# Kernel optimization log

Measured on AMD Instinct MI355X. Metric: run time of the kernel, lower is better.

## Reference

```python
import jax, jax.numpy as jnp
import numpy as np

WS = 8          # window size
DIM = 192
NH = 6          # num heads
HD = DIM // NH  # head dim = 32
HIDDEN = 768    # mlp_ratio 4
EPS = 1e-5


def _rel_tables(ws):
    # continuous relative-coords table, shape (1, 2w-1, 2w-1, 2)
    r = np.arange(-(ws - 1), ws, dtype=np.float32)
    table = np.stack(np.meshgrid(r, r, indexing='ij'), axis=-1)[None]
    table = table / (ws - 1) * 8.0
    # relative position index, shape (N, N)
    coords = np.stack(np.meshgrid(np.arange(ws), np.arange(ws), indexing='ij'))
    cf = coords.reshape(2, -1)
    rel = (cf[:, :, None] - cf[:, None, :]).transpose(1, 2, 0).astype(np.int64)
    rel[:, :, 0] += ws - 1
    rel[:, :, 1] += ws - 1
    rel[:, :, 0] *= 2 * ws - 1
    idx = rel.sum(-1)
    return jnp.asarray(table), jnp.asarray(idx)

_TABLE, _RPI = _rel_tables(WS)


def _layernorm(x, g, b):
    m = jnp.mean(x, -1, keepdims=True)
    v = jnp.var(x, -1, keepdims=True)
    return (x - m) * jax.lax.rsqrt(v + EPS) * g + b


def setup_inputs() -> dict:
    key = jax.random.key(0)
    ks = jax.random.split(key, 12)
    B, H, W = 2, 256, 256
    s = 0.02
    return {
        'x': jax.random.normal(ks[0], (B, H * W, DIM), jnp.float32),
        'scale': jax.random.uniform(ks[1], (1, 2), jnp.float32, 0.5, 2.0),
        'norm1_g': jnp.ones((DIM,), jnp.float32),
        'norm1_b': jnp.zeros((DIM,), jnp.float32),
        'qkv_w': jax.random.normal(ks[2], (DIM, 3 * DIM), jnp.float32) * s,
        'qkv_b': jnp.zeros((3 * DIM,), jnp.float32),
        'proj_w': jax.random.normal(ks[3], (DIM, DIM), jnp.float32) * s,
        'proj_b': jnp.zeros((DIM,), jnp.float32),
        'cpb_w1': jax.random.normal(ks[4], (4, 512), jnp.float32) * s,
        'cpb_b1': jnp.zeros((512,), jnp.float32),
        'cpb_w2': jax.random.normal(ks[5], (512, NH), jnp.float32) * s,
        'cpb_b2': jnp.zeros((NH,), jnp.float32),
        'norm2_g': jnp.ones((DIM,), jnp.float32),
        'norm2_b': jnp.zeros((DIM,), jnp.float32),
        'fc1_w': jax.random.normal(ks[6], (DIM, HIDDEN), jnp.float32) * s,
        'fc1_b': jnp.zeros((HIDDEN,), jnp.float32),
        'fc2_w': jax.random.normal(ks[7], (HIDDEN, DIM), jnp.float32) * s,
        'fc2_b': jnp.zeros((DIM,), jnp.float32),
        'dw_w': jax.random.normal(ks[8], (HIDDEN, 1, 3, 3), jnp.float32) * s,
        'dw_b': jnp.zeros((HIDDEN,), jnp.float32),
        'H': 256,
        'W': 256,
    }


def reference(x, scale, norm1_g, norm1_b, qkv_w, qkv_b, proj_w, proj_b,
              cpb_w1, cpb_b1, cpb_w2, cpb_b2, norm2_g, norm2_b,
              fc1_w, fc1_b, fc2_w, fc2_b, dw_w, dw_b, H, W):
    B, L, C = x.shape
    N = WS * WS
    shortcut = x

    # ---- W-MSA branch ----
    h = _layernorm(x, norm1_g, norm1_b).reshape(B, H, W, C)
    # window partition -> (B*nW, N, C)
    h = h.reshape(B, H // WS, WS, W // WS, WS, C).transpose(0, 1, 3, 2, 4, 5)
    xw = h.reshape(-1, N, C)
    B_ = xw.shape[0]

    qkv = (xw @ qkv_w + qkv_b).reshape(B_, N, 3, NH, HD).transpose(2, 0, 3, 1, 4)
    q, k, v = qkv[0], qkv[1], qkv[2]          # (B_, NH, N, HD)
    q = q * (HD ** -0.5)
    attn = jnp.einsum('bhnd,bhmd->bhnm', q, k)  # (B_, NH, N, N)

    # continuous relative position bias from cpb MLP conditioned on `scale`
    rel_cell = jnp.broadcast_to(scale[:, None, None, :], _TABLE.shape)  # (1,2w-1,2w-1,2)
    coords4 = jnp.concatenate([_TABLE, rel_cell], axis=-1)              # (1,2w-1,2w-1,4)
    bias_tab = (jax.nn.relu(coords4 @ cpb_w1 + cpb_b1) @ cpb_w2 + cpb_b2).reshape(-1, NH)
    rpb = bias_tab[_RPI.reshape(-1)].reshape(N, N, NH).transpose(2, 0, 1)  # (NH,N,N)
    attn = jax.nn.softmax(attn + rpb[None], axis=-1)

    out = jnp.einsum('bhnm,bhmd->bhnd', attn, v).transpose(0, 2, 1, 3).reshape(B_, N, C)
    out = out @ proj_w + proj_b

    # window reverse
    out = out.reshape(B, H // WS, W // WS, WS, WS, C).transpose(0, 1, 3, 2, 4, 5)
    out = out.reshape(B, L, C)
    x = shortcut + out

    # ---- conv-augmented MLP branch ----
    h = _layernorm(x, norm2_g, norm2_b)
    h = jax.nn.gelu(h @ fc1_w + fc1_b, approximate=False)   # (B, L, HIDDEN)
    hc = h.transpose(0, 2, 1).reshape(B, HIDDEN, H, W)
    hc = jax.lax.conv_general_dilated(
        hc, dw_w, window_strides=(1, 1), padding=((1, 1), (1, 1)),
        dimension_numbers=('NCHW', 'OIHW', 'NCHW'), feature_group_count=HIDDEN)
    hc = hc + dw_b[None, :, None, None]
    h = hc.reshape(B, HIDDEN, L).transpose(0, 2, 1)
    h = jax.nn.gelu(h, approximate=False)
    h = h @ fc2_w + fc2_b
    return x + h
```

## Files before the change

### kernel.cpp

```cpp
#include <hip/hip_runtime.h>
#include <hip/hip_bf16.h>

typedef __attribute__((ext_vector_type(8))) short  bf16x8;
typedef __attribute__((ext_vector_type(4))) float  f32x4;
typedef __attribute__((ext_vector_type(8))) unsigned short u16x8;
typedef __attribute__((ext_vector_type(4))) unsigned short u16x4;

__device__ __forceinline__ unsigned short f2b(float f) {
    unsigned int u = __builtin_bit_cast(unsigned int, f);
    u += 0x7FFFu + ((u >> 16) & 1u);
    return (unsigned short)(u >> 16);
}
__device__ __forceinline__ float b2f(unsigned short u) {
    return __builtin_bit_cast(float, (unsigned int)u << 16);
}
__device__ __forceinline__ float gelu_fast(float x) {
    float d = 1.0f + __expf(-1.702f * x);
    return x * __builtin_amdgcn_rcpf(d);
}
__device__ __forceinline__ int wperm(int m) {
    int w = m >> 6, n = m & 63;
    int b = w >> 10, wy = (w >> 5) & 31, wx = w & 31;
    int y = wy * 8 + (n >> 3), xx = wx * 8 + (n & 7);
    return (b << 16) + (y << 8) + xx;
}
__device__ __forceinline__ int wperm_inv(int r) {
    int rb = r >> 16, ry = (r >> 8) & 255, rx = r & 255;
    return (((rb << 10) + ((ry >> 3) << 5) + (rx >> 3)) << 6) + ((ry & 7) << 3) + (rx & 7);
}

__device__ __forceinline__ void gload_lds16(const void* g, void* l) {
    __builtin_amdgcn_global_load_lds(
        (const __attribute__((address_space(1))) void*)g,
        (__attribute__((address_space(3))) void*)l, 16, 0, 0);
}

__global__ void transpose_w(const float* __restrict__ in, unsigned short* __restrict__ out,
                            int K, int N) {
    int i = blockIdx.x * 256 + threadIdx.x;
    if (i >= K * N) return;
    int n = i / K, k = i - n * K;
    out[i] = f2b(in[k * N + n]);
}

__global__ void transpose_wf(const float* __restrict__ in, float* __restrict__ out,
                             int K, int N) {
    int i = blockIdx.x * 256 + threadIdx.x;
    if (i >= K * N) return;
    int n = i / K, k = i - n * K;
    out[i] = in[k * N + n];
}

__global__ __launch_bounds__(256) void cpb_kernel(
    const float* __restrict__ scale, const float* __restrict__ w1, const float* __restrict__ b1,
    const float* __restrict__ w2, const float* __restrict__ b2, float* __restrict__ btab) {
    int t = threadIdx.x;
    if (t >= 225) return;
    int i = t / 15, j = t - (t / 15) * 15;
    float ti = (i - 7) * (8.0f / 7.0f);
    float tj = (j - 7) * (8.0f / 7.0f);
    float s0 = scale[0], s1 = scale[1];
    float acc[6];
    #pragma unroll
    for (int h = 0; h < 6; ++h) acc[h] = b2[h];
    for (int k = 0; k < 512; ++k) {
        float hv = ti * w1[k] + tj * w1[512 + k] + s0 * w1[1024 + k] + s1 * w1[1536 + k] + b1[k];
        hv = fmaxf(hv, 0.f);
        #pragma unroll
        for (int h = 0; h < 6; ++h) acc[h] += hv * w2[k * 6 + h];
    }
    #pragma unroll
    for (int h = 0; h < 6; ++h) btab[t * 6 + h] = acc[h];
}

__global__ __launch_bounds__(256) void ln_full(
    const float* __restrict__ xin, const float* __restrict__ g, const float* __restrict__ b,
    unsigned short* __restrict__ ow) {
    int r = blockIdx.x * 4 + (threadIdx.x >> 6);
    int lane = threadIdx.x & 63;
    const float* p = xin + (size_t)r * 192;
    float a0 = p[lane], a1 = p[lane + 64], a2 = p[lane + 128];
    float s = a0 + a1 + a2;
    float q = a0 * a0 + a1 * a1 + a2 * a2;
    #pragma unroll
    for (int off = 1; off < 64; off <<= 1) {
        s += __shfl_xor(s, off);
        q += __shfl_xor(q, off);
    }
    float mean = s * (1.f / 192.f);
    float rstd = rsqrtf(q * (1.f / 192.f) - mean * mean + 1e-5f);
    unsigned short* o = ow + (size_t)wperm_inv(r) * 192;
    o[lane]       = f2b((a0 - mean) * rstd * g[lane] + b[lane]);
    o[lane + 64]  = f2b((a1 - mean) * rstd * g[lane + 64] + b[lane + 64]);
    o[lane + 128] = f2b((a2 - mean) * rstd * g[lane + 128] + b[lane + 128]);
}

template<int MODE>
__global__ __launch_bounds__(256) void gemm192(
    const float* __restrict__ Af, const unsigned short* __restrict__ Ab,
    const float* __restrict__ stats, const float* __restrict__ lng, const float* __restrict__ lnb,
    const unsigned short* __restrict__ Bt, const float* __restrict__ bias,
    unsigned short* __restrict__ oq, unsigned short* __restrict__ ok2, unsigned short* __restrict__ ov,
    const float* __restrict__ resid, float* __restrict__ ofp, unsigned short* __restrict__ obf,
    float* __restrict__ ostat) {
    __shared__ __align__(16) unsigned short Asw[2 * 128 * 64];
    __shared__ __align__(16) unsigned short Bsw[2 * 192 * 64];
    const int t = threadIdx.x;
    const int lane = t & 63;
    const int wv = t >> 6, wm = wv >> 1, wn = wv & 1;
    const int n0 = blockIdx.x * 192;
    const int m0 = blockIdx.y * 128;
    const int l15 = lane & 15, lq = lane >> 4;

    int aoffs[4], boffs[6];
    if constexpr (MODE != 2) {
        #pragma unroll
        for (int s = 0; s < 4; ++s) {
            int row = (wv + 4 * s) * 8 + (lane >> 3);
            aoffs[s] = (m0 + row) * 192 + (((lane & 7) ^ (lane >> 3)) * 8);
        }
    }
    #pragma unroll
    for (int s = 0; s < 6; ++s) {
        int row = (wv + 4 * s) * 8 + (lane >> 3);
        boffs[s] = (n0 + row) * 192 + (((lane & 7) ^ (lane >> 3)) * 8);
    }

    f32x4 acc[4][6];
    #pragma unroll
    for (int i = 0; i < 4; ++i)
        #pragma unroll
        for (int j = 0; j < 6; ++j) acc[i][j] = (f32x4){0.f, 0.f, 0.f, 0.f};

    if constexpr (MODE != 2) {
        #pragma unroll
        for (int s = 0; s < 4; ++s)
            gload_lds16(Ab + aoffs[s], (char*)Asw + (wv + 4 * s) * 1024);
    }
    #pragma unroll
    for (int s = 0; s < 6; ++s)
        gload_lds16(Bt + boffs[s], (char*)Bsw + (wv + 4 * s) * 1024);

    int cur = 0;
    const int axor = (l15 & 7) << 4;
    for (int c = 0; c < 3; ++c) {
        const int k0 = c * 64;
        if (c < 2) {
            if constexpr (MODE != 2) {
                #pragma unroll
                for (int s = 0; s < 4; ++s)
                    gload_lds16(Ab + aoffs[s] + k0 + 64,
                                (char*)Asw + (cur ^ 1) * 16384 + (wv + 4 * s) * 1024);
            }
            #pragma unroll
            for (int s = 0; s < 6; ++s)
                gload_lds16(Bt + boffs[s] + k0 + 64,
                            (char*)Bsw + (cur ^ 1) * 24576 + (wv + 4 * s) * 1024);
        }
        if constexpr (MODE == 2) {
            #pragma unroll
            for (int i = 0; i < 8; ++i) {
                int c2 = t + i * 256;
                int row = c2 >> 4, ch = c2 & 15;
                int m = m0 + row;
                f32x4 v = *(const f32x4*)(Af + (size_t)m * 192 + k0 + ch * 4);
                float mean = stats[2 * m], rstd = stats[2 * m + 1];
                u16x4 pk;
                #pragma unroll
                for (int j = 0; j < 4; ++j) {
                    int kk = k0 + ch * 4 + j;
                    pk[j] = f2b((v[j] - mean) * rstd * lng[kk] + lnb[kk]);
                }
                int byte = row * 128 + ((((ch >> 1) ^ (row & 7)) << 4) + ((ch & 1) << 3));
                *(u16x4*)((char*)Asw + byte) = pk;
            }
            asm volatile("s_waitcnt lgkmcnt(0)" ::: "memory");
        }
        if (c < 2) {
            if constexpr (MODE == 2) asm volatile("s_waitcnt vmcnt(6)" ::: "memory");
            else                     asm volatile("s_waitcnt vmcnt(10)" ::: "memory");
        } else {
            asm volatile("s_waitcnt vmcnt(0)" ::: "memory");
        }
        __builtin_amdgcn_s_barrier();
        __builtin_amdgcn_sched_barrier(0);
        const char* Al = (const char*)Asw + ((MODE == 2) ? 0 : cur * 16384);
        const char* Bl = (const char*)Bsw + cur * 24576;
        #pragma unroll
        for (int kk = 0; kk < 2; ++kk) {
            bf16x8 a[4], bb[6];
            #pragma unroll
            for (int mt = 0; mt < 4; ++mt)
                a[mt] = *(const bf16x8*)(Al + (wm * 64 + mt * 16 + l15) * 128 +
                                         ((kk << 6) ^ (lq << 4) ^ axor));
            #pragma unroll
            for (int nt = 0; nt < 6; ++nt)
                bb[nt] = *(const bf16x8*)(Bl + (wn * 96 + nt * 16 + l15) * 128 +
                                          ((kk << 6) ^ (lq << 4) ^ axor));
            #pragma unroll
            for (int mt = 0; mt < 4; ++mt)
                #pragma unroll
                for (int nt = 0; nt < 6; ++nt)
                    acc[mt][nt] = __builtin_amdgcn_mfma_f32_16x16x32_bf16(a[mt], bb[nt], acc[mt][nt], 0, 0, 0);
        }
        __builtin_amdgcn_sched_barrier(0);
        __builtin_amdgcn_s_barrier();
        __builtin_amdgcn_sched_barrier(0);
        cur ^= 1;
    }

    if constexpr (MODE == 1) {
        float* ls  = (float*)Asw;
        float* lsq = ls + 256;
        #pragma unroll
        for (int mt = 0; mt < 4; ++mt) {
            #pragma unroll
            for (int r = 0; r < 4; ++r) {
                int lrow = wm * 64 + mt * 16 + lq * 4 + r;
                int m = m0 + lrow;
                int r2 = wperm(m);
                float s = 0.f, q = 0.f;
                #pragma unroll
                for (int nt = 0; nt < 6; ++nt) {
                    int c = wn * 96 + nt * 16 + l15;
                    size_t idx = (size_t)r2 * 192 + c;
                    float w = resid[idx] + acc[mt][nt][r] + bias[c];
                    ofp[idx] = w;
                    s += w;
                    q += w * w;
                }
                #pragma unroll
                for (int off = 1; off < 16; off <<= 1) {
                    s += __shfl_xor(s, off);
                    q += __shfl_xor(q, off);
                }
                if (l15 == 0) {
                    ls[lrow * 2 + wn] = s;
                    lsq[lrow * 2 + wn] = q;
                }
            }
        }
        __syncthreads();
        if (t < 128) {
            float s = ls[t * 2] + ls[t * 2 + 1];
            float q = lsq[t * 2] + lsq[t * 2 + 1];
            float mean = s * (1.f / 192.f);
            float var = q * (1.f / 192.f) - mean * mean;
            int r2 = wperm(m0 + t);
            ostat[2 * r2] = mean;
            ostat[2 * r2 + 1] = rsqrtf(var + 1e-5f);
        }
    } else {
        #pragma unroll
        for (int mt = 0; mt < 4; ++mt) {
            #pragma unroll
            for (int nt = 0; nt < 6; ++nt) {
                #pragma unroll
                for (int r = 0; r < 4; ++r) {
                    int m = m0 + wm * 64 + mt * 16 + lq * 4 + r;
                    int c = n0 + wn * 96 + nt * 16 + l15;
                    float v = acc[mt][nt][r] + bias[c];
                    if constexpr (MODE == 0) {
                        int which = c / 192;
                        int head = (c % 192) >> 5;
                        int d = c & 31;
                        int w = m >> 6, n = m & 63;
                        unsigned short* dst = (which == 0) ? oq : (which == 1) ? ok2 : ov;
                        if (which == 0) v *= 0.17677669529663689f;
                        dst[((size_t)(w * 6 + head) * 64 + n) * 32 + d] = f2b(v);
                    } else {
                        obf[(size_t)m * 768 + c] = f2b(gelu_fast(v));
                    }
                }
            }
        }
    }
}

__global__ __launch_bounds__(64) void attn_win(
    const unsigned short* __restrict__ qb, const unsigned short* __restrict__ kb,
    const unsigned short* __restrict__ vb, const float* __restrict__ btab,
    unsigned short* __restrict__ ao) {
    __shared__ float sb[225];
    __shared__ __align__(16) unsigned short pl[64 * 72];
    __shared__ __align__(16) unsigned short vT[32 * 72];
    const int bid = blockIdx.x;
    const int w = bid / 6, h = bid - w * 6;
    const int lane = threadIdx.x;
    const int l15 = lane & 15, lq = lane >> 4;

    for (int i = lane; i < 225; i += 64) sb[i] = btab[i * 6 + h];

    const unsigned short* qp = qb + (size_t)bid * 2048;
    const unsigned short* kp = kb + (size_t)bid * 2048;
    const unsigned short* vp = vb + (size_t)bid * 2048;

    bf16x8 qf[4], kf[4];
    #pragma unroll
    for (int i = 0; i < 4; ++i) {
        qf[i] = *(const bf16x8*)(qp + (i * 16 + l15) * 32 + lq * 8);
        kf[i] = *(const bf16x8*)(kp + (i * 16 + l15) * 32 + lq * 8);
    }
    #pragma unroll
    for (int i = 0; i < 4; ++i) {
        int c = lane + i * 64;
        int mr = c >> 2, d0 = (c & 3) * 8;
        u16x8 v = *(const u16x8*)(vp + mr * 32 + d0);
        #pragma unroll
        for (int j = 0; j < 8; ++j) vT[(d0 + j) * 72 + mr] = v[j];
    }
    f32x4 s[4][4];
    #pragma unroll
    for (int mt = 0; mt < 4; ++mt)
        #pragma unroll
        for (int nt = 0; nt < 4; ++nt)
            s[mt][nt] = __builtin_amdgcn_mfma_f32_16x16x32_bf16(
                qf[mt], kf[nt], (f32x4){0.f, 0.f, 0.f, 0.f}, 0, 0, 0);
    __syncthreads();
    #pragma unroll
    for (int mt = 0; mt < 4; ++mt) {
        #pragma unroll
        for (int r = 0; r < 4; ++r) {
            int n = mt * 16 + lq * 4 + r;
            int ny = n >> 3, nx = n & 7;
            float sv[4];
            float mx = -1e30f;
            #pragma unroll
            for (int nt = 0; nt < 4; ++nt) {
                int m = nt * 16 + l15;
                int idx = (ny - (m >> 3) + 7) * 15 + (nx - (m & 7) + 7);
                float val = s[mt][nt][r] + sb[idx];
                sv[nt] = val;
                mx = fmaxf(mx, val);
            }
            #pragma unroll
            for (int off = 1; off < 16; off <<= 1) mx = fmaxf(mx, __shfl_xor(mx, off));
            float sum = 0.f;
            #pragma unroll
            for (int nt = 0; nt < 4; ++nt) { sv[nt] = __expf(sv[nt] - mx); sum += sv[nt]; }
            #pragma unroll
            for (int off = 1; off < 16; off <<= 1) sum += __shfl_xor(sum, off);
            float inv = 1.f / sum;
            #pragma unroll
            for (int nt = 0; nt < 4; ++nt)
                pl[n * 72 + nt * 16 + l15] = f2b(sv[nt] * inv);
        }
    }
    __syncthreads();
    f32x4 o[4][2];
    #pragma unroll
    for (int i = 0; i < 4; ++i)
        #pragma unroll
        for (int j = 0; j < 2; ++j) o[i][j] = (f32x4){0.f, 0.f, 0.f, 0.f};
    #pragma unroll
    for (int mt = 0; mt < 4; ++mt)
        #pragma unroll
        for (int kk = 0; kk < 2; ++kk) {
            bf16x8 a = *(bf16x8*)&pl[(mt * 16 + l15) * 72 + kk * 32 + lq * 8];
            #pragma unroll
            for (int dt = 0; dt < 2; ++dt) {
                bf16x8 b = *(bf16x8*)&vT[(dt * 16 + l15) * 72 + kk * 32 + lq * 8];
                o[mt][dt] = __builtin_amdgcn_mfma_f32_16x16x32_bf16(a, b, o[mt][dt], 0, 0, 0);
            }
        }
    #pragma unroll
    for (int mt = 0; mt < 4; ++mt)
        #pragma unroll
        for (int dt = 0; dt < 2; ++dt)
            #pragma unroll
            for (int r = 0; r < 4; ++r) {
                int n = mt * 16 + lq * 4 + r;
                int d = dt * 16 + l15;
                ao[((size_t)w * 64 + n) * 192 + h * 32 + d] = f2b(o[mt][dt][r]);
            }
}

__global__ __launch_bounds__(512) void conv_fc2_v12(
    const unsigned short* __restrict__ m1, const float* __restrict__ dwwTf,
    const float* __restrict__ dwb, const unsigned short* __restrict__ fc2T,
    const float* __restrict__ fc2b, float* __restrict__ out) {
    __shared__ __align__(16) unsigned short Xs[4 * 34 * 64];
    __shared__ __align__(16) unsigned short As[64 * 72];
    __shared__ __align__(16) unsigned short Bsw[192 * 64];
    const int t = threadIdx.x;
    const int g = ((blockIdx.x & 7) << 8) + (blockIdx.x >> 3);
    const int b = g >> 10, ypair = (g >> 3) & 127, xq = g & 7;
    const int y0 = ypair * 2, x0 = xq * 32;
    const int cg = t & 7, lx = t >> 3;
    const int ix = lx & 31, iy = lx >> 5;
    const size_t ibase = (size_t)b * 65536;

    const int lane = t & 63, wv8 = t >> 6;
    const int wm = wv8 >> 2, wn = wv8 & 3;
    const int l15 = lane & 15, lq = lane >> 4;

    int xoff[3];
    #pragma unroll
    for (int s = 0; s < 3; ++s) {
        int seg = (s < 2) ? (wv8 + 8 * s) : 16;
        int p = seg * 8 + (lane >> 3);
        int ry = p / 34, px = p - ry * 34;
        int gy = min(max(y0 - 1 + ry, 0), 255);
        int gx = min(max(x0 - 1 + px, 0), 255);
        xoff[s] = ((b << 16) + (gy << 8) + gx) * 768 + (lane & 7) * 8;
    }
    int boff[3];
    #pragma unroll
    for (int s = 0; s < 3; ++s) {
        int row = (wv8 + 8 * s) * 8 + (lane >> 3);
        boff[s] = row * 768 + ((lane & 7) ^ (lane >> 3)) * 8;
    }

    f32x4 acc[2][3];
    #pragma unroll
    for (int i = 0; i < 2; ++i)
        #pragma unroll
        for (int j = 0; j < 3; ++j) acc[i][j] = (f32x4){0.f, 0.f, 0.f, 0.f};

    #pragma unroll
    for (int s = 0; s < 3; ++s)
        if (s < 2 || wv8 == 0)
            gload_lds16(m1 + xoff[s], (char*)Xs + (((s < 2) ? (wv8 + 8 * s) : 16)) * 1024);
    #pragma unroll
    for (int s = 0; s < 3; ++s)
        gload_lds16(fc2T + boff[s], (char*)Bsw + (wv8 + 8 * s) * 1024);

    const int xb = ix * 128 + cg * 16;
    const int gxp = x0 + ix;
    const bool xok0 = gxp >= 1;
    const bool xok2 = gxp <= 254;
    const int oy = y0 + iy;
    const int o00 = (lq * 16) ^ ((l15 & 7) << 4);
    const int brow = (wn * 48 + l15) * 128;

    for (int k0 = 0; k0 < 768; k0 += 64) {
        const int c0 = k0 + cg * 8;
        asm volatile("s_waitcnt vmcnt(0)" ::: "memory");
        __syncthreads();
        float a[8];
        #pragma unroll
        for (int j = 0; j < 8; ++j) a[j] = 0.f;
        #pragma unroll
        for (int ky = 0; ky < 3; ++ky) {
            if ((unsigned)(oy + ky - 1) >= 256u) continue;
            #pragma unroll
            for (int kx = 0; kx < 3; ++kx) {
                if (kx == 0 && !xok0) continue;
                if (kx == 2 && !xok2) continue;
                const float* wp = dwwTf + (ky * 3 + kx) * 768 + c0;
                f32x4 w0 = *(const f32x4*)wp;
                f32x4 w1 = *(const f32x4*)(wp + 4);
                u16x8 in = *(const u16x8*)((const char*)Xs + (iy + ky) * 4352 + xb + kx * 128);
                #pragma unroll
                for (int j = 0; j < 4; ++j) {
                    a[j]     += b2f(in[j]) * w0[j];
                    a[4 + j] += b2f(in[4 + j]) * w1[j];
                }
            }
        }
        {
            f32x4 b0 = *(const f32x4*)(dwb + c0);
            f32x4 b1 = *(const f32x4*)(dwb + c0 + 4);
            u16x8 o;
            #pragma unroll
            for (int j = 0; j < 4; ++j) {
                o[j]     = f2b(gelu_fast(a[j] + b0[j]));
                o[4 + j] = f2b(gelu_fast(a[4 + j] + b1[j]));
            }
            *(u16x8*)&As[lx * 72 + cg * 8] = o;
        }
        __syncthreads();
        if (k0 < 704) {
            #pragma unroll
            for (int s = 0; s < 3; ++s)
                if (s < 2 || wv8 == 0)
                    gload_lds16(m1 + xoff[s] + k0 + 64,
                                (char*)Xs + (((s < 2) ? (wv8 + 8 * s) : 16)) * 1024);
        }
        #pragma unroll
        for (int kk = 0; kk < 2; ++kk) {
            bf16x8 af[2];
            #pragma unroll
            for (int mt = 0; mt < 2; ++mt)
                af[mt] = *(bf16x8*)&As[(wm * 32 + mt * 16 + l15) * 72 + kk * 32 + lq * 8];
            #pragma unroll
            for (int nt = 0; nt < 3; ++nt) {
                bf16x8 bb = *(const bf16x8*)((const char*)Bsw + brow + nt * 2048 + (o00 ^ (kk << 6)));
                #pragma unroll
                for (int mt = 0; mt < 2; ++mt)
                    acc[mt][nt] = __builtin_amdgcn_mfma_f32_16x16x32_bf16(af[mt], bb, acc[mt][nt], 0, 0, 0);
            }
        }
        __syncthreads();
        if (k0 < 704) {
            #pragma unroll
            for (int s = 0; s < 3; ++s)
                gload_lds16(fc2T + boff[s] + k0 + 64, (char*)Bsw + (wv8 + 8 * s) * 1024);
        }
    }
    #pragma unroll
    for (int mt = 0; mt < 2; ++mt)
        #pragma unroll
        for (int nt = 0; nt < 3; ++nt)
            #pragma unroll
            for (int r = 0; r < 4; ++r) {
                int ml = wm * 32 + mt * 16 + lq * 4 + r;
                int py = ml >> 5, lxx = ml & 31;
                int col = wn * 48 + nt * 16 + l15;
                size_t idx = (ibase + (size_t)(y0 + py) * 256 + x0 + lxx) * 192 + col;
                out[idx] = out[idx] + acc[mt][nt][r] + fc2b[col];
            }
}

extern "C" void kernel_launch(void* const* d_in, const int* in_sizes, int n_in,
                              void* d_out, int out_size, void* d_ws, size_t ws_size,
                              hipStream_t stream) {
    (void)in_sizes; (void)n_in; (void)out_size; (void)ws_size;
    const float* x     = (const float*)d_in[0];
    const float* scale = (const float*)d_in[1];
    const float* n1g   = (const float*)d_in[2];
    const float* n1b   = (const float*)d_in[3];
    const float* qkvw  = (const float*)d_in[4];
    const float* qkvb  = (const float*)d_in[5];
    const float* projw = (const float*)d_in[6];
    const float* projb = (const float*)d_in[7];
    const float* cw1   = (const float*)d_in[8];
    const float* cb1   = (const float*)d_in[9];
    const float* cw2   = (const float*)d_in[10];
    const float* cb2   = (const float*)d_in[11];
    const float* n2g   = (const float*)d_in[12];
    const float* n2b   = (const float*)d_in[13];
    const float* fc1w  = (const float*)d_in[14];
    const float* fc1b  = (const float*)d_in[15];
    const float* fc2w  = (const float*)d_in[16];
    const float* fc2b  = (const float*)d_in[17];
    const float* dww   = (const float*)d_in[18];
    const float* dwb   = (const float*)d_in[19];
    float* out = (float*)d_out;

    char* ws = (char*)d_ws;
    unsigned short* qkvT  = (unsigned short*)ws;
    unsigned short* projT = qkvT + 110592;
    unsigned short* fc1T  = projT + 36864;
    unsigned short* fc2T  = fc1T + 147456;
    float* btab   = (float*)(ws + 1048576);
    float* dwwTf  = (float*)(ws + 1310720);
    float* stats  = (float*)(ws + 2097152);
    unsigned short* pool = (unsigned short*)(ws + 4194304);
    const size_t S = 25165824;
    unsigned short* qb = pool;
    unsigned short* kb = pool + S;
    unsigned short* vb = pool + 2 * S;
    unsigned short* ab = pool + 3 * S;
    unsigned short* m1 = pool;
    unsigned short* xnw = (unsigned short*)d_out;

    transpose_w<<<432, 256, 0, stream>>>(qkvw, qkvT, 192, 576);
    transpose_w<<<144, 256, 0, stream>>>(projw, projT, 192, 192);
    transpose_w<<<576, 256, 0, stream>>>(fc1w, fc1T, 192, 768);
    transpose_w<<<576, 256, 0, stream>>>(fc2w, fc2T, 768, 192);
    transpose_wf<<<27, 256, 0, stream>>>(dww, dwwTf, 768, 9);
    cpb_kernel<<<1, 256, 0, stream>>>(scale, cw1, cb1, cw2, cb2, btab);

    ln_full<<<32768, 256, 0, stream>>>(x, n1g, n1b, xnw);
    gemm192<0><<<dim3(3, 1024), 256, 0, stream>>>(
        (const float*)nullptr, xnw, (const float*)nullptr, (const float*)nullptr,
        (const float*)nullptr, qkvT, qkvb,
        qb, kb, vb, (const float*)nullptr, (float*)nullptr, (unsigned short*)nullptr,
        (float*)nullptr);
    attn_win<<<12288, 64, 0, stream>>>(qb, kb, vb, btab, ab);
    gemm192<1><<<dim3(1, 1024), 256, 0, stream>>>(
        (const float*)nullptr, ab, (const float*)nullptr, (const float*)nullptr,
        (const float*)nullptr, projT, projb,
        (unsigned short*)nullptr, (unsigned short*)nullptr, (unsigned short*)nullptr,
        x, out, (unsigned short*)nullptr, stats);
    gemm192<2><<<dim3(4, 1024), 256, 0, stream>>>(
        out, (const unsigned short*)nullptr, stats, n2g, n2b, fc1T, fc1b,
        (unsigned short*)nullptr, (unsigned short*)nullptr, (unsigned short*)nullptr,
        (const float*)nullptr, (float*)nullptr, m1, (float*)nullptr);
    conv_fc2_v12<<<2048, 512, 0, stream>>>(m1, dwwTf, dwb, fc2T, fc2b, out);
}
```

Baseline: 633.1 us.

## Keep A tile resident and loop over N tiles; read fc2 weights from global

The GEMM kernel is restructured so each block owns 64 rows with the full K=192 A tile held in LDS, and loops over all 192-wide column tiles internally. This replaces the 128x192 block grid that reloaded A (and recomputed LayerNorm for the fc1 GEMM) once per column tile. B tiles are double-buffered across a flattened column/k loop. Separately, the conv+fc2 kernel drops its LDS staging of fc2 weights and loads B fragments straight from global/L2, removing barriers and LDS traffic but relying on cache hits for the weight reads.

```diff
diff --git a/kernel.cpp b/kernel.cpp
--- a/kernel.cpp
+++ b/kernel.cpp
@@ -96,182 +96,178 @@
 }
 
 template<int MODE>
-__global__ __launch_bounds__(256) void gemm192(
+__global__ __launch_bounds__(256) void gemm64(
     const float* __restrict__ Af, const unsigned short* __restrict__ Ab,
     const float* __restrict__ stats, const float* __restrict__ lng, const float* __restrict__ lnb,
     const unsigned short* __restrict__ Bt, const float* __restrict__ bias,
     unsigned short* __restrict__ oq, unsigned short* __restrict__ ok2, unsigned short* __restrict__ ov,
     const float* __restrict__ resid, float* __restrict__ ofp, unsigned short* __restrict__ obf,
     float* __restrict__ ostat) {
-    __shared__ __align__(16) unsigned short Asw[2 * 128 * 64];
+    constexpr int NCT = (MODE == 0) ? 3 : (MODE == 2) ? 4 : 1;
+    __shared__ __align__(16) unsigned short Asw[3 * 64 * 64];
     __shared__ __align__(16) unsigned short Bsw[2 * 192 * 64];
-    const int t = threadIdx.x;
-    const int lane = t & 63;
-    const int wv = t >> 6, wm = wv >> 1, wn = wv & 1;
-    const int n0 = blockIdx.x * 192;
-    const int m0 = blockIdx.y * 128;
+    const int t = threadIdx.x, lane = t & 63, wv = t >> 6;
+    const int wm = wv >> 1, wn = wv & 1;
     const int l15 = lane & 15, lq = lane >> 4;
-
-    int aoffs[4], boffs[6];
-    if constexpr (MODE != 2) {
-        #pragma unroll
-        for (int s = 0; s < 4; ++s) {
-            int row = (wv + 4 * s) * 8 + (lane >> 3);
-            aoffs[s] = (m0 + row) * 192 + (((lane & 7) ^ (lane >> 3)) * 8);
-        }
-    }
+    const int m0 = blockIdx.x * 64;
+
+    int boffs[6];
     #pragma unroll
     for (int s = 0; s < 6; ++s) {
         int row = (wv + 4 * s) * 8 + (lane >> 3);
-        boffs[s] = (n0 + row) * 192 + (((lane & 7) ^ (lane >> 3)) * 8);
-    }
-
-    f32x4 acc[4][6];
-    #pragma unroll
-    for (int i = 0; i < 4; ++i)
-        #pragma unroll
-        for (int j = 0; j < 6; ++j) acc[i][j] = (f32x4){0.f, 0.f, 0.f, 0.f};
-
+        boffs[s] = row * 192 + ((lane & 7) ^ (lane >> 3)) * 8;
+    }
     if constexpr (MODE != 2) {
         #pragma unroll
-        for (int s = 0; s < 4; ++s)
-            gload_lds16(Ab + aoffs[s], (char*)Asw + (wv + 4 * s) * 1024);
+        for (int s = 0; s < 6; ++s) {
+            int si = wv + 4 * s;
+            int row = (si & 7) * 8 + (lane >> 3);
+            int src = (m0 + row) * 192 + (si >> 3) * 64 + ((lane & 7) ^ (lane >> 3)) * 8;
+            gload_lds16(Ab + src, (char*)Asw + si * 1024);
+        }
     }
     #pragma unroll
     for (int s = 0; s < 6; ++s)
         gload_lds16(Bt + boffs[s], (char*)Bsw + (wv + 4 * s) * 1024);
 
-    int cur = 0;
-    const int axor = (l15 & 7) << 4;
-    for (int c = 0; c < 3; ++c) {
-        const int k0 = c * 64;
-        if (c < 2) {
-            if constexpr (MODE != 2) {
-                #pragma unroll
-                for (int s = 0; s < 4; ++s)
-                    gload_lds16(Ab + aoffs[s] + k0 + 64,
-                                (char*)Asw + (cur ^ 1) * 16384 + (wv + 4 * s) * 1024);
-            }
-            #pragma unroll
-            for (int s = 0; s < 6; ++s)
-                gload_lds16(Bt + boffs[s] + k0 + 64,
-                            (char*)Bsw + (cur ^ 1) * 24576 + (wv + 4 * s) * 1024);
-        }
-        if constexpr (MODE == 2) {
-            #pragma unroll
-            for (int i = 0; i < 8; ++i) {
+    if constexpr (MODE == 2) {
+        #pragma unroll
+        for (int c = 0; c < 3; ++c) {
+            #pragma unroll
+            for (int i = 0; i < 4; ++i) {
                 int c2 = t + i * 256;
                 int row = c2 >> 4, ch = c2 & 15;
                 int m = m0 + row;
-                f32x4 v = *(const f32x4*)(Af + (size_t)m * 192 + k0 + ch * 4);
+                f32x4 v = *(const f32x4*)(Af + (size_t)m * 192 + c * 64 + ch * 4);
                 float mean = stats[2 * m], rstd = stats[2 * m + 1];
                 u16x4 pk;
                 #pragma unroll
                 for (int j = 0; j < 4; ++j) {
-                    int kk = k0 + ch * 4 + j;
+                    int kk = c * 64 + ch * 4 + j;
                     pk[j] = f2b((v[j] - mean) * rstd * lng[kk] + lnb[kk]);
                 }
-                int byte = row * 128 + ((((ch >> 1) ^ (row & 7)) << 4) + ((ch & 1) << 3));
+                int byte = c * 8192 + row * 128 +
+                           ((((ch >> 1) ^ (row & 7)) << 4) + ((ch & 1) << 3));
                 *(u16x4*)((char*)Asw + byte) = pk;
             }
-            asm volatile("s_waitcnt lgkmcnt(0)" ::: "memory");
-        }
-        if (c < 2) {
-            if constexpr (MODE == 2) asm volatile("s_waitcnt vmcnt(6)" ::: "memory");
-            else                     asm volatile("s_waitcnt vmcnt(10)" ::: "memory");
+        }
+        asm volatile("s_waitcnt lgkmcnt(0)" ::: "memory");
+    }
+
+    const int axor = (l15 & 7) << 4;
+    int cur = 0, it = 0;
+    for (int ct = 0; ct < NCT; ++ct) {
+        f32x4 acc[2][6];
+        #pragma unroll
+        for (int i = 0; i < 2; ++i)
+            #pragma unroll
+            for (int j = 0; j < 6; ++j) acc[i][j] = (f32x4){0.f, 0.f, 0.f, 0.f};
+        for (int c = 0; c < 3; ++c, ++it) {
+            if (it < NCT * 3 - 1) {
+                int ctn = (c == 2) ? ct + 1 : ct;
+                int cn  = (c == 2) ? 0 : c + 1;
+                #pragma unroll
+                for (int s = 0; s < 6; ++s)
+                    gload_lds16(Bt + (size_t)ctn * 36864 + boffs[s] + cn * 64,
+                                (char*)Bsw + (cur ^ 1) * 24576 + (wv + 4 * s) * 1024);
+                asm volatile("s_waitcnt vmcnt(6)" ::: "memory");
+            } else {
+                asm volatile("s_waitcnt vmcnt(0)" ::: "memory");
+            }
+            __builtin_amdgcn_sched_barrier(0);
+            __builtin_amdgcn_s_barrier();
+            __builtin_amdgcn_sched_barrier(0);
+            const char* Al = (const char*)Asw + c * 8192;
+            const char* Bl = (const char*)Bsw + cur * 24576;
+            #pragma unroll
+            for (int kk = 0; kk < 2; ++kk) {
+                bf16x8 a[2], bb[6];
+                #pragma unroll
+                for (int mt = 0; mt < 2; ++mt)
+                    a[mt] = *(const bf16x8*)(Al + (wm * 32 + mt * 16 + l15) * 128 +
+                                             ((kk << 6) ^ (lq << 4) ^ axor));
+                #pragma unroll
+                for (int nt = 0; nt < 6; ++nt)
+                    bb[nt] = *(const bf16x8*)(Bl + (wn * 96 + nt * 16 + l15) * 128 +
+                                              ((kk << 6) ^ (lq << 4) ^ axor));
+                #pragma unroll
+                for (int mt = 0; mt < 2; ++mt)
+                    #pragma unroll
+                    for (int nt = 0; nt < 6; ++nt)
+                        acc[mt][nt] = __builtin_amdgcn_mfma_f32_16x16x32_bf16(a[mt], bb[nt], acc[mt][nt], 0, 0, 0);
+            }
+            __builtin_amdgcn_sched_barrier(0);
+            __builtin_amdgcn_s_barrier();
+            cur ^= 1;
+        }
+        if constexpr (MODE == 0) {
+            unsigned short* dst = (ct == 0) ? oq : (ct == 1) ? ok2 : ov;
+            float qs = (ct == 0) ? 0.17677669529663689f : 1.0f;
+            #pragma unroll
+            for (int mt = 0; mt < 2; ++mt)
+                #pragma unroll
+                for (int nt = 0; nt < 6; ++nt)
+                    #pragma unroll
+                    for (int r = 0; r < 4; ++r) {
+                        int m = m0 + wm * 32 + mt * 16 + lq * 4 + r;
+                        int col = wn * 96 + nt * 16 + l15;
+                        float v = (acc[mt][nt][r] + bias[ct * 192 + col]) * qs;
+                        int head = col >> 5, d = col & 31;
+                        int w = m >> 6, n = m & 63;
+                        dst[((size_t)(w * 6 + head) * 64 + n) * 32 + d] = f2b(v);
+                    }
+        } else if constexpr (MODE == 2) {
+            #pragma unroll
+            for (int mt = 0; mt < 2; ++mt)
+                #pragma unroll
+                for (int nt = 0; nt < 6; ++nt)
+                    #pragma unroll
+                    for (int r = 0; r < 4; ++r) {
+                        int m = m0 + wm * 32 + mt * 16 + lq * 4 + r;
+                        int col = wn * 96 + nt * 16 + l15;
+                        obf[(size_t)m * 768 + ct * 192 + col] =
+                            f2b(gelu_fast(acc[mt][nt][r] + bias[ct * 192 + col]));
+                    }
         } else {
-            asm volatile("s_waitcnt vmcnt(0)" ::: "memory");
-        }
-        __builtin_amdgcn_s_barrier();
-        __builtin_amdgcn_sched_barrier(0);
-        const char* Al = (const char*)Asw + ((MODE == 2) ? 0 : cur * 16384);
-        const char* Bl = (const char*)Bsw + cur * 24576;
-        #pragma unroll
-        for (int kk = 0; kk < 2; ++kk) {
-            bf16x8 a[4], bb[6];
-            #pragma unroll
-            for (int mt = 0; mt < 4; ++mt)
-                a[mt] = *(const bf16x8*)(Al + (wm * 64 + mt * 16 + l15) * 128 +
-                                         ((kk << 6) ^ (lq << 4) ^ axor));
-            #pragma unroll
-            for (int nt = 0; nt < 6; ++nt)
-                bb[nt] = *(const bf16x8*)(Bl + (wn * 96 + nt * 16 + l15) * 128 +
-                                          ((kk << 6) ^ (lq << 4) ^ axor));
-            #pragma unroll
-            for (int mt = 0; mt < 4; ++mt)
-                #pragma unroll
-                for (int nt = 0; nt < 6; ++nt)
-                    acc[mt][nt] = __builtin_amdgcn_mfma_f32_16x16x32_bf16(a[mt], bb[nt], acc[mt][nt], 0, 0, 0);
-        }
-        __builtin_amdgcn_sched_barrier(0);
-        __builtin_amdgcn_s_barrier();
-        __builtin_amdgcn_sched_barrier(0);
-        cur ^= 1;
-    }
-
-    if constexpr (MODE == 1) {
-        float* ls  = (float*)Asw;
-        float* lsq = ls + 256;
-        #pragma unroll
-        for (int mt = 0; mt < 4; ++mt) {
-            #pragma unroll
-            for (int r = 0; r < 4; ++r) {
-                int lrow = wm * 64 + mt * 16 + lq * 4 + r;
-                int m = m0 + lrow;
-                int r2 = wperm(m);
-                float s = 0.f, q = 0.f;
-                #pragma unroll
-                for (int nt = 0; nt < 6; ++nt) {
-                    int c = wn * 96 + nt * 16 + l15;
-                    size_t idx = (size_t)r2 * 192 + c;
-                    float w = resid[idx] + acc[mt][nt][r] + bias[c];
-                    ofp[idx] = w;
-                    s += w;
-                    q += w * w;
-                }
-                #pragma unroll
-                for (int off = 1; off < 16; off <<= 1) {
-                    s += __shfl_xor(s, off);
-                    q += __shfl_xor(q, off);
-                }
-                if (l15 == 0) {
-                    ls[lrow * 2 + wn] = s;
-                    lsq[lrow * 2 + wn] = q;
-                }
-            }
-        }
-        __syncthreads();
-        if (t < 128) {
-            float s = ls[t * 2] + ls[t * 2 + 1];
-            float q = lsq[t * 2] + lsq[t * 2 + 1];
-            float mean = s * (1.f / 192.f);
-            float var = q * (1.f / 192.f) - mean * mean;
-            int r2 = wperm(m0 + t);
-            ostat[2 * r2] = mean;
-            ostat[2 * r2 + 1] = rsqrtf(var + 1e-5f);
-        }
-    } else {
-        #pragma unroll
-        for (int mt = 0; mt < 4; ++mt) {
-            #pragma unroll
-            for (int nt = 0; nt < 6; ++nt) {
+            float* ls  = (float*)Asw;
+            float* lsq = ls + 128;
+            #pragma unroll
+            for (int mt = 0; mt < 2; ++mt) {
                 #pragma unroll
                 for (int r = 0; r < 4; ++r) {
-                    int m = m0 + wm * 64 + mt * 16 + lq * 4 + r;
-                    int c = n0 + wn * 96 + nt * 16 + l15;
-                    float v = acc[mt][nt][r] + bias[c];
-                    if constexpr (MODE == 0) {
-                        int which = c / 192;
-                        int head = (c % 192) >> 5;
-                        int d = c & 31;
-                        int w = m >> 6, n = m & 63;
-                        unsigned short* dst = (which == 0) ? oq : (which == 1) ? ok2 : ov;
-                        if (which == 0) v *= 0.17677669529663689f;
-                        dst[((size_t)(w * 6 + head) * 64 + n) * 32 + d] = f2b(v);
-                    } else {
-                        obf[(size_t)m * 768 + c] = f2b(gelu_fast(v));
+                    int lrow = wm * 32 + mt * 16 + lq * 4 + r;
+                    int m = m0 + lrow;
+                    int r2 = wperm(m);
+                    float s = 0.f, q = 0.f;
+                    #pragma unroll
+                    for (int nt = 0; nt < 6; ++nt) {
+                        int col = wn * 96 + nt * 16 + l15;
+                        size_t idx = (size_t)r2 * 192 + col;
+                        float w = resid[idx] + acc[mt][nt][r] + bias[col];
+                        ofp[idx] = w;
+                        s += w;
+                        q += w * w;
+                    }
+                    #pragma unroll
+                    for (int off = 1; off < 16; off <<= 1) {
+                        s += __shfl_xor(s, off);
+                        q += __shfl_xor(q, off);
+                    }
+                    if (l15 == 0) {
+                        ls[lrow * 2 + wn] = s;
+                        lsq[lrow * 2 + wn] = q;
                     }
                 }
+            }
+            __syncthreads();
+            if (t < 64) {
+                float s = ls[t * 2] + ls[t * 2 + 1];
+                float q = lsq[t * 2] + lsq[t * 2 + 1];
+                float mean = s * (1.f / 192.f);
+                float var = q * (1.f / 192.f) - mean * mean;
+                int r2 = wperm(m0 + t);
+                ostat[2 * r2] = mean;
+                ostat[2 * r2 + 1] = rsqrtf(var + 1e-5f);
             }
         }
     }
@@ -375,13 +371,12 @@
             }
 }
 
-__global__ __launch_bounds__(512) void conv_fc2_v12(
+__global__ __launch_bounds__(512) void conv_fc2_v13(
     const unsigned short* __restrict__ m1, const float* __restrict__ dwwTf,
     const float* __restrict__ dwb, const unsigned short* __restrict__ fc2T,
     const float* __restrict__ fc2b, float* __restrict__ out) {
     __shared__ __align__(16) unsigned short Xs[4 * 34 * 64];
     __shared__ __align__(16) unsigned short As[64 * 72];
-    __shared__ __align__(16) unsigned short Bsw[192 * 64];
     const int t = threadIdx.x;
     const int g = ((blockIdx.x & 7) << 8) + (blockIdx.x >> 3);
     const int b = g >> 10, ypair = (g >> 3) & 127, xq = g & 7;
@@ -404,12 +399,6 @@
         int gx = min(max(x0 - 1 + px, 0), 255);
         xoff[s] = ((b << 16) + (gy << 8) + gx) * 768 + (lane & 7) * 8;
     }
-    int boff[3];
-    #pragma unroll
-    for (int s = 0; s < 3; ++s) {
-        int row = (wv8 + 8 * s) * 8 + (lane >> 3);
-        boff[s] = row * 768 + ((lane & 7) ^ (lane >> 3)) * 8;
-    }
 
     f32x4 acc[2][3];
     #pragma unroll
@@ -421,17 +410,13 @@
     for (int s = 0; s < 3; ++s)
         if (s < 2 || wv8 == 0)
             gload_lds16(m1 + xoff[s], (char*)Xs + (((s < 2) ? (wv8 + 8 * s) : 16)) * 1024);
-    #pragma unroll
-    for (int s = 0; s < 3; ++s)
-        gload_lds16(fc2T + boff[s], (char*)Bsw + (wv8 + 8 * s) * 1024);
 
     const int xb = ix * 128 + cg * 16;
     const int gxp = x0 + ix;
     const bool xok0 = gxp >= 1;
     const bool xok2 = gxp <= 254;
     const int oy = y0 + iy;
-    const int o00 = (lq * 16) ^ ((l15 & 7) << 4);
-    const int brow = (wn * 48 + l15) * 128;
+    const unsigned short* fcb = fc2T + (size_t)(wn * 48 + l15) * 768 + lq * 8;
 
     for (int k0 = 0; k0 < 768; k0 += 64) {
         const int c0 = k0 + cg * 8;
@@ -485,17 +470,11 @@
                 af[mt] = *(bf16x8*)&As[(wm * 32 + mt * 16 + l15) * 72 + kk * 32 + lq * 8];
             #pragma unroll
             for (int nt = 0; nt < 3; ++nt) {
-                bf16x8 bb = *(const bf16x8*)((const char*)Bsw + brow + nt * 2048 + (o00 ^ (kk << 6)));
+                bf16x8 bb = *(const bf16x8*)(fcb + nt * 16 * 768 + k0 + kk * 32);
                 #pragma unroll
                 for (int mt = 0; mt < 2; ++mt)
                     acc[mt][nt] = __builtin_amdgcn_mfma_f32_16x16x32_bf16(af[mt], bb, acc[mt][nt], 0, 0, 0);
             }
-        }
-        __syncthreads();
-        if (k0 < 704) {
-            #pragma unroll
-            for (int s = 0; s < 3; ++s)
-                gload_lds16(fc2T + boff[s] + k0 + 64, (char*)Bsw + (wv8 + 8 * s) * 1024);
         }
     }
     #pragma unroll
@@ -563,20 +542,20 @@
     cpb_kernel<<<1, 256, 0, stream>>>(scale, cw1, cb1, cw2, cb2, btab);
 
     ln_full<<<32768, 256, 0, stream>>>(x, n1g, n1b, xnw);
-    gemm192<0><<<dim3(3, 1024), 256, 0, stream>>>(
+    gemm64<0><<<2048, 256, 0, stream>>>(
         (const float*)nullptr, xnw, (const float*)nullptr, (const float*)nullptr,
         (const float*)nullptr, qkvT, qkvb,
         qb, kb, vb, (const float*)nullptr, (float*)nullptr, (unsigned short*)nullptr,
         (float*)nullptr);
     attn_win<<<12288, 64, 0, stream>>>(qb, kb, vb, btab, ab);
-    gemm192<1><<<dim3(1, 1024), 256, 0, stream>>>(
+    gemm64<1><<<2048, 256, 0, stream>>>(
         (const float*)nullptr, ab, (const float*)nullptr, (const float*)nullptr,
         (const float*)nullptr, projT, projb,
         (unsigned short*)nullptr, (unsigned short*)nullptr, (unsigned short*)nullptr,
         x, out, (unsigned short*)nullptr, stats);
-    gemm192<2><<<dim3(4, 1024), 256, 0, stream>>>(
+    gemm64<2><<<2048, 256, 0, stream>>>(
         out, (const unsigned short*)nullptr, stats, n2g, n2b, fc1T, fc1b,
         (unsigned short*)nullptr, (unsigned short*)nullptr, (unsigned short*)nullptr,
         (const float*)nullptr, (float*)nullptr, m1, (float*)nullptr);
-    conv_fc2_v12<<<2048, 512, 0, stream>>>(m1, dwwTf, dwb, fc2T, fc2b, out);
-}
+    conv_fc2_v13<<<2048, 512, 0, stream>>>(m1, dwwTf, dwb, fc2T, fc2b, out);
+}
```

Result: slower. 690.4 us (+9.1%).
